# Optimization experiments

Hardware: AMD Instinct MI355X
Metric: run time of the kernel (lower is better)

Reference implementation:

```python
import jax, jax.numpy as jnp
import numpy as np

NHEAD = 8
HEAD_DIM = 32
AREA_WIDTH = 4
H = 32   # coarse grid height (hw0_c == hw1_c, agg_scale already applied)
W = 40   # coarse grid width
C_MAX = max(H, W) * AREA_WIDTH  # max_candidate_num = 160


def _skew(t):
    # t: [N,3] -> [N,3,3] cross-product matrix
    z = jnp.zeros_like(t[:, 0])
    return jnp.stack([
        jnp.stack([z, -t[:, 2], t[:, 1]], -1),
        jnp.stack([t[:, 2], z, -t[:, 0]], -1),
        jnp.stack([-t[:, 1], t[:, 0], z], -1),
    ], -2)


def _candidate_info(K0, K1, R, t):
    # Pixel coords in (x, y) order, as kornia.create_meshgrid(..., normalized=False)
    ys, xs = jnp.meshgrid(jnp.arange(H, dtype=jnp.float32),
                          jnp.arange(W, dtype=jnp.float32), indexing='ij')
    coord = jnp.stack([xs, ys], -1).reshape(-1, 2)  # [S,2]
    S = coord.shape[0]
    # Fundamental matrix F = K1^{-T} [t]_x R K0^{-1}
    F = jnp.swapaxes(jnp.linalg.inv(K1), -1, -2) @ _skew(t) @ R @ jnp.linalg.inv(K0)
    p = jnp.concatenate([coord, jnp.ones((S, 1), jnp.float32)], -1)  # [S,3] homogeneous
    lines = jnp.einsum('nij,lj->nli', F, p)  # [N,L,3] epipolar lines a*u+b*v+c=0 in image1
    a, b, c = lines[..., 0], lines[..., 1], lines[..., 2]
    mode = jnp.abs(b) > jnp.abs(a)  # True: parametrize v = f(u); False: u = f(v)
    b_safe = jnp.where(mode, b, 1.0)
    a_safe = jnp.where(mode, 1.0, a)
    # v(u) band check
    coord_y = (-a / b_safe)[..., None] * coord[:, 0] + (-c / b_safe)[..., None]  # [N,L,S]
    within_y = (coord[:, 1] < coord_y + AREA_WIDTH / 2.0) & (coord[:, 1] > coord_y - AREA_WIDTH / 2.0)
    # u(v) band check
    coord_x = (-b / a_safe)[..., None] * coord[:, 1] + (-c / a_safe)[..., None]  # [N,L,S]
    within_x = (coord[:, 0] < coord_x + AREA_WIDTH / 2.0) & (coord[:, 0] > coord_x - AREA_WIDTH / 2.0)
    within = jnp.where(mode[..., None], within_y, within_x)  # [N,L,S]
    # gather_index: keep the C_MAX largest source indices whose mask bit is set
    idx = jnp.arange(S)
    true_idx = jnp.where(within, idx, 0)           # [N,L,S]
    true_idx = jnp.sort(true_idx, axis=-1)
    c_index = true_idx[..., -C_MAX:]               # [N,L,C]
    valid = c_index != 0                           # index 0 treated as invalid (as in original)
    return c_index, valid


def setup_inputs() -> dict:
    key = jax.random.key(0)
    kq, kk, kv = jax.random.split(key, 3)
    N = 1
    feat = NHEAD * HEAD_DIM
    query = jax.random.normal(kq, (N, H, W, feat), jnp.float32)
    key_t = jax.random.normal(kk, (N, H, W, feat), jnp.float32)
    value = jax.random.normal(kv, (N, H, W, feat), jnp.float32)
    f = 35.0
    Kmat = jnp.array([[[f, 0.0, W / 2.0], [0.0, f, H / 2.0], [0.0, 0.0, 1.0]]], jnp.float32)
    R = jnp.eye(3, dtype=jnp.float32)[None]
    t = jnp.array([[1.0, 0.15, 0.02]], jnp.float32)
    return {"query": query, "key": key_t, "value": value, "K0": Kmat, "K1": Kmat, "R": R, "t": t}


def reference(query, key, value, K0, K1, R, t):
    c_index, valid = _candidate_info(K0, K1, R, t)  # [N,L,C] int / bool (no-grad constants)
    N = query.shape[0]
    L = H * W
    q = query.reshape(N, L, NHEAD, HEAD_DIM)
    k = key.reshape(N, L, NHEAD, HEAD_DIM)
    v = value.reshape(N, L, NHEAD, HEAD_DIM)
    n_idx = jnp.arange(N)[:, None, None]
    k_g = k[n_idx, c_index]  # [N,L,C,nhead,d]
    v_g = v[n_idx, c_index]  # [N,L,C,nhead,d]
    qk = jnp.einsum('nlhd,nlchd->nlch', q, k_g)
    scale = 1.0 / jnp.sqrt(jnp.float32(HEAD_DIM))
    scores = jnp.where(valid[..., None], qk * scale, -jnp.inf)
    A = jnp.nan_to_num(jax.nn.softmax(scores, axis=2), nan=0.0)  # fully-masked rows -> 0
    return jnp.einsum('nlch,nlchd->nlhd', A, v_g)  # [N,L,nhead,d]
```

## Files before the change

kernel.cpp:

```cpp
#include <hip/hip_runtime.h>
#include <math.h>

#define NHEAD 8
#define HEAD_DIM 32
#define IMG_H 32
#define IMG_W 40
#define NPIX (IMG_H*IMG_W)
#define CMAX 160
#define NITER (CMAX/8)
#define FEAT (NHEAD*HEAD_DIM)


__device__ void np_inv3x3_f32(const float* M, float inv[3][3]) {
#pragma clang fp contract(off)
    float A[3][3]; int piv[3];
    for (int i=0;i<3;i++) { A[i][0]=M[i*3+0]; A[i][1]=M[i*3+1]; A[i][2]=M[i*3+2]; }
    for (int kk=0;kk<3;kk++) {
        int p = kk;
        float colmax = fabsf(A[kk][kk]);
        for (int i=kk+1;i<3;i++) { float vv=fabsf(A[i][kk]); if (vv>colmax){colmax=vv;p=i;} }
        piv[kk] = p;
        if (p!=kk) { for(int j=0;j<3;j++){float tmp=A[kk][j];A[kk][j]=A[p][j];A[p][j]=tmp;} }
        const float rp = 1.0f / A[kk][kk];
        for (int i=kk+1;i<3;i++) A[i][kk] = A[i][kk] * rp;
        for (int i=kk+1;i<3;i++)
            for (int j=kk+1;j<3;j++)
                A[i][j] = A[i][j] - A[i][kk]*A[kk][j];
    }
    for (int col=0; col<3; col++) {
        float b[3] = {0.f,0.f,0.f}; b[col] = 1.0f;
        for (int kk=0;kk<3;kk++) if (piv[kk]!=kk) { float tmp=b[kk]; b[kk]=b[piv[kk]]; b[piv[kk]]=tmp; }
        for (int i=1;i<3;i++)
            for (int kk=0;kk<i;kk++)
                b[i] = b[i] - A[i][kk]*b[kk];
        for (int kk=2;kk>=0;kk--) {
            b[kk] = b[kk] / A[kk][kk];
            for (int i=0;i<kk;i++)
                b[i] = b[i] - A[i][kk]*b[kk];
        }
        inv[0][col]=b[0]; inv[1][col]=b[1]; inv[2][col]=b[2];
    }
}

__device__ void mm3_chain(const float A[3][3], const float B[3][3], float C[3][3]) {
#pragma clang fp contract(off)
    for (int i=0;i<3;i++)
        for (int j=0;j<3;j++) {
            float acc = A[i][0]*B[0][j];
            acc = acc + A[i][1]*B[1][j];
            acc = acc + A[i][2]*B[2][j];
            C[i][j] = acc;
        }
}
__device__ void mm3_fma(const float A[3][3], const float B[3][3], float C[3][3]) {
#pragma clang fp contract(off)
    for (int i=0;i<3;i++)
        for (int j=0;j<3;j++) {
            float acc = A[i][0]*B[0][j];
            acc = __builtin_fmaf(A[i][1], B[1][j], acc);
            acc = __builtin_fmaf(A[i][2], B[2][j], acc);
            C[i][j] = acc;
        }
}
__device__ float einsum_row(const float Fi[3], float x, float y) {
#pragma clang fp contract(off)
    float acc = Fi[0]*x;
    acc = acc + Fi[1]*y;
    acc = acc + Fi[2]*1.0f;
    return acc;
}

__global__ __launch_bounds__(64) void geo_kernel(
    const float* __restrict__ K0, const float* __restrict__ K1,
    const float* __restrict__ R, const float* __restrict__ t,
    float4* __restrict__ geo)
{
#pragma clang fp contract(off)
    const int l = blockIdx.x * 64 + threadIdx.x;
    float i0[3][3], i1[3][3], A[3][3], B[3][3], T1[3][3], T2[3][3], F[3][3], Rm[3][3];
    np_inv3x3_f32(K0, i0);
    np_inv3x3_f32(K1, i1);
    for (int i=0;i<3;i++)
        for (int j=0;j<3;j++) { A[i][j] = i1[j][i]; Rm[i][j] = R[i*3+j]; }
    const float t0=t[0], t1=t[1], t2=t[2];
    B[0][0]=0.f;  B[0][1]=-t2;  B[0][2]=t1;
    B[1][0]=t2;   B[1][1]=0.f;  B[1][2]=-t0;
    B[2][0]=-t1;  B[2][1]=t0;   B[2][2]=0.f;
    mm3_chain(A,B,T1);
    mm3_chain(T1,Rm,T2);
    mm3_fma(T2,i0,F);

    const float xl = (float)(l % IMG_W);
    const float yl = (float)(l / IMG_W);
    const float la = einsum_row(F[0], xl, yl);
    const float lb = einsum_row(F[1], xl, yl);
    const float lc = einsum_row(F[2], xl, yl);
    const bool  mode  = fabsf(lb) > fabsf(la);
    const float denom = mode ? lb : la;
    const float slope = (mode ? -la : -lb) / denom;
    const float icpt  = (-lc) / denom;
    geo[l] = make_float4(slope, icpt, mode ? 1.0f : 0.0f, 0.0f);
}


__global__ __launch_bounds__(512) void one2many_attn(
    const float* __restrict__ q, const float* __restrict__ k, const float* __restrict__ v,
    const float4* __restrict__ geo, float* __restrict__ out)
{
#pragma clang fp contract(off)
    __shared__ int s_cand[CMAX];
    __shared__ int s_cnt;

    const int bx  = blockIdx.x;
    const int l   = (bx >> 3) + (bx & 7) * 160;
    const int tid = threadIdx.x;

    if (tid == 0) s_cnt = 0;

    const float4 g = geo[l];
    const float slope = g.x;
    const float icpt  = g.y;
    const bool  mode  = (g.z != 0.0f);

    const int h    = tid >> 6;
    const int lane = tid & 63;
    const int grp  = lane >> 3;
    const int dj   = (lane & 7) << 2;

    const float4 q4 = *(const float4*)(q + l*FEAT + h*HEAD_DIM + dj);

    __syncthreads();

    for (int m = tid; m < NPIX; m += 512) {
        const float xm = (float)(m % IMG_W), ym = (float)(m / IMG_W);
        const float tin  = mode ? xm : ym;
        const float tchk = mode ? ym : xm;
        const float mu = slope * tin;
        const float cc = mu + icpt;
        const float hi = cc + 2.0f;
        const float lo = cc - 2.0f;
        if ((tchk < hi) && (tchk > lo) && m != 0) {
            int pos = atomicAdd(&s_cnt, 1);
            if (pos < CMAX) s_cand[pos] = m;
        }
    }
    __syncthreads();
    const int nc = min(s_cnt, CMAX);

    const float* kh = k + h*HEAD_DIM + dj;
    const float* vh = v + h*HEAD_DIM + dj;

    float ax = 0.f, ay = 0.f, az = 0.f, aw = 0.f, ps = 0.f;
    #pragma unroll
    for (int i = 0; i < NITER; i++) {
        const int ci  = (i << 3) + grp;
        const int row = s_cand[(ci < nc) ? ci : 0];
        const size_t off = (size_t)row * FEAT;
        const float4 kk = *(const float4*)(kh + off);
        const float4 vv = *(const float4*)(vh + off);
        float p = q4.x*kk.x;
        p = __builtin_fmaf(q4.y, kk.y, p);
        p = __builtin_fmaf(q4.z, kk.z, p);
        p = __builtin_fmaf(q4.w, kk.w, p);
        p += __shfl_xor(p, 1);
        p += __shfl_xor(p, 2);
        p += __shfl_xor(p, 4);
        const float e = (ci < nc) ? __expf(p * 0.17677669529663687f) : 0.0f;
        ps += e;
        ax = __builtin_fmaf(e, vv.x, ax);
        ay = __builtin_fmaf(e, vv.y, ay);
        az = __builtin_fmaf(e, vv.z, az);
        aw = __builtin_fmaf(e, vv.w, aw);
    }

    #pragma unroll
    for (int o = 8; o <= 32; o <<= 1) {
        ax += __shfl_xor(ax, o);
        ay += __shfl_xor(ay, o);
        az += __shfl_xor(az, o);
        aw += __shfl_xor(aw, o);
        ps += __shfl_xor(ps, o);
    }

    if (lane < 8) {
        float4 r;
        if (nc > 0) { r.x = ax/ps; r.y = ay/ps; r.z = az/ps; r.w = aw/ps; }
        else        { r.x = r.y = r.z = r.w = 0.0f; }
        *(float4*)(out + l*FEAT + h*HEAD_DIM + dj) = r;
    }
}

extern "C" void kernel_launch(void* const* d_in, const int* in_sizes, int n_in,
                              void* d_out, int out_size, void* d_ws, size_t ws_size,
                              hipStream_t stream) {
    const float* q  = (const float*)d_in[0];
    const float* k  = (const float*)d_in[1];
    const float* v  = (const float*)d_in[2];
    const float* K0 = (const float*)d_in[3];
    const float* K1 = (const float*)d_in[4];
    const float* R  = (const float*)d_in[5];
    const float* t  = (const float*)d_in[6];
    float* out = (float*)d_out;
    float4* geo = (float4*)d_ws;
    geo_kernel<<<NPIX/64, 64, 0, stream>>>(K0, K1, R, t, geo);
    one2many_attn<<<NPIX, 512, 0, stream>>>(q, k, v, geo, out);
}
```

Measured before the change: 89.77 us.

## Fuse epipolar geometry into attention kernel and widen per-lane head slice

Removes the separate geo_kernel launch and instead computes the fundamental matrix and epipolar line parameters redundantly in every thread of the attention kernel. It also changes the thread mapping so each lane handles 8 head-dim elements instead of 4, with 16 candidate groups per wavefront instead of 8. This halves the loop iterations and cuts one shuffle stage in the dot-product reduction. The cost is redundant 3x3 inversions and matrix products per thread and more registers per thread.

```diff
diff --git a/kernel.cpp b/kernel.cpp
--- a/kernel.cpp
+++ b/kernel.cpp
@@ -7,7 +7,7 @@
 #define IMG_W 40
 #define NPIX (IMG_H*IMG_W)
 #define CMAX 160
-#define NITER (CMAX/8)
+#define NITER16 (CMAX/16)
 #define FEAT (NHEAD*HEAD_DIM)
 
 
@@ -70,64 +70,55 @@
     return acc;
 }
 
-__global__ __launch_bounds__(64) void geo_kernel(
+
+__global__ __launch_bounds__(512) void one2many_fused(
+    const float* __restrict__ q, const float* __restrict__ k, const float* __restrict__ v,
     const float* __restrict__ K0, const float* __restrict__ K1,
     const float* __restrict__ R, const float* __restrict__ t,
-    float4* __restrict__ geo)
-{
-#pragma clang fp contract(off)
-    const int l = blockIdx.x * 64 + threadIdx.x;
-    float i0[3][3], i1[3][3], A[3][3], B[3][3], T1[3][3], T2[3][3], F[3][3], Rm[3][3];
-    np_inv3x3_f32(K0, i0);
-    np_inv3x3_f32(K1, i1);
-    for (int i=0;i<3;i++)
-        for (int j=0;j<3;j++) { A[i][j] = i1[j][i]; Rm[i][j] = R[i*3+j]; }
-    const float t0=t[0], t1=t[1], t2=t[2];
-    B[0][0]=0.f;  B[0][1]=-t2;  B[0][2]=t1;
-    B[1][0]=t2;   B[1][1]=0.f;  B[1][2]=-t0;
-    B[2][0]=-t1;  B[2][1]=t0;   B[2][2]=0.f;
-    mm3_chain(A,B,T1);
-    mm3_chain(T1,Rm,T2);
-    mm3_fma(T2,i0,F);
-
-    const float xl = (float)(l % IMG_W);
-    const float yl = (float)(l / IMG_W);
-    const float la = einsum_row(F[0], xl, yl);
-    const float lb = einsum_row(F[1], xl, yl);
-    const float lc = einsum_row(F[2], xl, yl);
-    const bool  mode  = fabsf(lb) > fabsf(la);
-    const float denom = mode ? lb : la;
-    const float slope = (mode ? -la : -lb) / denom;
-    const float icpt  = (-lc) / denom;
-    geo[l] = make_float4(slope, icpt, mode ? 1.0f : 0.0f, 0.0f);
-}
-
-
-__global__ __launch_bounds__(512) void one2many_attn(
-    const float* __restrict__ q, const float* __restrict__ k, const float* __restrict__ v,
-    const float4* __restrict__ geo, float* __restrict__ out)
+    float* __restrict__ out)
 {
 #pragma clang fp contract(off)
     __shared__ int s_cand[CMAX];
     __shared__ int s_cnt;
 
-    const int bx  = blockIdx.x;
-    const int l   = (bx >> 3) + (bx & 7) * 160;
+    const int bxi = blockIdx.x;
+    const int l   = (bxi >> 3) + (bxi & 7) * 160;
     const int tid = threadIdx.x;
 
     if (tid == 0) s_cnt = 0;
-
-    const float4 g = geo[l];
-    const float slope = g.x;
-    const float icpt  = g.y;
-    const bool  mode  = (g.z != 0.0f);
 
     const int h    = tid >> 6;
     const int lane = tid & 63;
-    const int grp  = lane >> 3;
-    const int dj   = (lane & 7) << 2;
-
-    const float4 q4 = *(const float4*)(q + l*FEAT + h*HEAD_DIM + dj);
+    const int grp  = lane >> 2;
+    const int dj   = (lane & 3) << 3;
+
+    const float4 qa = *(const float4*)(q + l*FEAT + h*HEAD_DIM + dj);
+    const float4 qb = *(const float4*)(q + l*FEAT + h*HEAD_DIM + dj + 4);
+
+    float slope, icpt; bool mode;
+    {
+        float i0[3][3], i1[3][3], A[3][3], B[3][3], T1[3][3], T2[3][3], Fm[3][3], Rm[3][3];
+        np_inv3x3_f32(K0, i0);
+        np_inv3x3_f32(K1, i1);
+        for (int i=0;i<3;i++)
+            for (int j=0;j<3;j++) { A[i][j] = i1[j][i]; Rm[i][j] = R[i*3+j]; }
+        const float t0=t[0], t1=t[1], t2=t[2];
+        B[0][0]=0.f;  B[0][1]=-t2;  B[0][2]=t1;
+        B[1][0]=t2;   B[1][1]=0.f;  B[1][2]=-t0;
+        B[2][0]=-t1;  B[2][1]=t0;   B[2][2]=0.f;
+        mm3_chain(A,B,T1);
+        mm3_chain(T1,Rm,T2);
+        mm3_fma(T2,i0,Fm);
+        const float xl = (float)(l % IMG_W);
+        const float yl = (float)(l / IMG_W);
+        const float la = einsum_row(Fm[0], xl, yl);
+        const float lb = einsum_row(Fm[1], xl, yl);
+        const float lc = einsum_row(Fm[2], xl, yl);
+        mode = fabsf(lb) > fabsf(la);
+        const float denom = mode ? lb : la;
+        slope = (mode ? -la : -lb) / denom;
+        icpt  = (-lc) / denom;
+    }
 
     __syncthreads();
 
@@ -150,43 +141,64 @@
     const float* kh = k + h*HEAD_DIM + dj;
     const float* vh = v + h*HEAD_DIM + dj;
 
-    float ax = 0.f, ay = 0.f, az = 0.f, aw = 0.f, ps = 0.f;
+    float4 aA = make_float4(0.f,0.f,0.f,0.f);
+    float4 aB = make_float4(0.f,0.f,0.f,0.f);
+    float ps = 0.f;
     #pragma unroll
-    for (int i = 0; i < NITER; i++) {
-        const int ci  = (i << 3) + grp;
+    for (int i = 0; i < NITER16; i++) {
+        const int ci  = (i << 4) + grp;
         const int row = s_cand[(ci < nc) ? ci : 0];
         const size_t off = (size_t)row * FEAT;
-        const float4 kk = *(const float4*)(kh + off);
-        const float4 vv = *(const float4*)(vh + off);
-        float p = q4.x*kk.x;
-        p = __builtin_fmaf(q4.y, kk.y, p);
-        p = __builtin_fmaf(q4.z, kk.z, p);
-        p = __builtin_fmaf(q4.w, kk.w, p);
+        const float4 ka = *(const float4*)(kh + off);
+        const float4 kb = *(const float4*)(kh + off + 4);
+        const float4 va = *(const float4*)(vh + off);
+        const float4 vb = *(const float4*)(vh + off + 4);
+        float p = qa.x*ka.x;
+        p = __builtin_fmaf(qa.y, ka.y, p);
+        p = __builtin_fmaf(qa.z, ka.z, p);
+        p = __builtin_fmaf(qa.w, ka.w, p);
+        p = __builtin_fmaf(qb.x, kb.x, p);
+        p = __builtin_fmaf(qb.y, kb.y, p);
+        p = __builtin_fmaf(qb.z, kb.z, p);
+        p = __builtin_fmaf(qb.w, kb.w, p);
         p += __shfl_xor(p, 1);
         p += __shfl_xor(p, 2);
-        p += __shfl_xor(p, 4);
         const float e = (ci < nc) ? __expf(p * 0.17677669529663687f) : 0.0f;
         ps += e;
-        ax = __builtin_fmaf(e, vv.x, ax);
-        ay = __builtin_fmaf(e, vv.y, ay);
-        az = __builtin_fmaf(e, vv.z, az);
-        aw = __builtin_fmaf(e, vv.w, aw);
+        aA.x = __builtin_fmaf(e, va.x, aA.x);
+        aA.y = __builtin_fmaf(e, va.y, aA.y);
+        aA.z = __builtin_fmaf(e, va.z, aA.z);
+        aA.w = __builtin_fmaf(e, va.w, aA.w);
+        aB.x = __builtin_fmaf(e, vb.x, aB.x);
+        aB.y = __builtin_fmaf(e, vb.y, aB.y);
+        aB.z = __builtin_fmaf(e, vb.z, aB.z);
+        aB.w = __builtin_fmaf(e, vb.w, aB.w);
     }
 
     #pragma unroll
-    for (int o = 8; o <= 32; o <<= 1) {
-        ax += __shfl_xor(ax, o);
-        ay += __shfl_xor(ay, o);
-        az += __shfl_xor(az, o);
-        aw += __shfl_xor(aw, o);
-        ps += __shfl_xor(ps, o);
-    }
-
-    if (lane < 8) {
-        float4 r;
-        if (nc > 0) { r.x = ax/ps; r.y = ay/ps; r.z = az/ps; r.w = aw/ps; }
-        else        { r.x = r.y = r.z = r.w = 0.0f; }
-        *(float4*)(out + l*FEAT + h*HEAD_DIM + dj) = r;
+    for (int o = 4; o <= 32; o <<= 1) {
+        aA.x += __shfl_xor(aA.x, o);
+        aA.y += __shfl_xor(aA.y, o);
+        aA.z += __shfl_xor(aA.z, o);
+        aA.w += __shfl_xor(aA.w, o);
+        aB.x += __shfl_xor(aB.x, o);
+        aB.y += __shfl_xor(aB.y, o);
+        aB.z += __shfl_xor(aB.z, o);
+        aB.w += __shfl_xor(aB.w, o);
+        ps   += __shfl_xor(ps, o);
+    }
+
+    if (lane < 4) {
+        float4 rA, rB;
+        if (nc > 0) {
+            rA.x = aA.x/ps; rA.y = aA.y/ps; rA.z = aA.z/ps; rA.w = aA.w/ps;
+            rB.x = aB.x/ps; rB.y = aB.y/ps; rB.z = aB.z/ps; rB.w = aB.w/ps;
+        } else {
+            rA.x = rA.y = rA.z = rA.w = 0.0f;
+            rB.x = rB.y = rB.z = rB.w = 0.0f;
+        }
+        *(float4*)(out + l*FEAT + h*HEAD_DIM + dj)     = rA;
+        *(float4*)(out + l*FEAT + h*HEAD_DIM + dj + 4) = rB;
     }
 }
 
@@ -201,7 +213,6 @@
     const float* R  = (const float*)d_in[5];
     const float* t  = (const float*)d_in[6];
     float* out = (float*)d_out;
-    float4* geo = (float4*)d_ws;
-    geo_kernel<<<NPIX/64, 64, 0, stream>>>(K0, K1, R, t, geo);
-    one2many_attn<<<NPIX, 512, 0, stream>>>(q, k, v, geo, out);
-}
+    (void)d_ws; (void)ws_size;
+    one2many_fused<<<NPIX, 512, 0, stream>>>(q, k, v, K0, K1, R, t, out);
+}
```

New measurement: 118.7 us. 1.32x slower.
